# Kernel tuning notes

Measured on AMD Instinct MI355X. Metric: run time of the kernel, lower is better.

## Reference

```python
import jax, jax.numpy as jnp
import numpy as np

IN_FEATURES = 256
NUM_CENTERS = 4096
BATCH = 16384
SIGMA = 1.0


def setup_inputs() -> dict:
    key = jax.random.key(0)
    kx, kc, kw, kb = jax.random.split(key, 4)
    x = jax.random.normal(kx, (BATCH, IN_FEATURES), dtype=jnp.float32)
    centers = jax.random.normal(kc, (NUM_CENTERS, IN_FEATURES), dtype=jnp.float32)
    # nn.Linear(num_centers, 1) default init: U(-1/sqrt(fan_in), 1/sqrt(fan_in))
    bound = 1.0 / np.sqrt(NUM_CENTERS)
    w = jax.random.uniform(kw, (1, NUM_CENTERS), dtype=jnp.float32, minval=-bound, maxval=bound)
    b = jax.random.uniform(kb, (1,), dtype=jnp.float32, minval=-bound, maxval=bound)
    return {"x": x, "centers": centers, "w": w, "b": b}


def reference(x, centers, w, b):
    x_sq = jnp.sum(x * x, axis=1, keepdims=True)          # [B, 1]
    c_sq = jnp.sum(centers * centers, axis=1)             # [C]
    cross = jnp.einsum('bf,cf->bc', x, centers)           # [B, C]
    dist = x_sq + c_sq[None, :] - 2.0 * cross             # [B, C]
    phi = jnp.exp(-dist / (2.0 * SIGMA ** 2))             # [B, C]
    out = phi @ w.T + b                                   # [B, 1]
    return jax.nn.sigmoid(out)
```

## Files before the change

kernel.cpp:

```cpp
#include <hip/hip_runtime.h>
#include <hip/hip_bf16.h>


#define BATCH 16384
#define NCENT 4096
#define KDIM  256

using i32x4 = __attribute__((ext_vector_type(4))) int;

#define AS1 __attribute__((address_space(1)))
#define AS3 __attribute__((address_space(3)))
#define GLOAD_LDS16(g, l) \
  __builtin_amdgcn_global_load_lds((const AS1 void*)(g), (AS3 void*)(l), 16, 0, 0)

__device__ __forceinline__ unsigned short f2bf(float f) {
  unsigned int u = __float_as_uint(f);
  return (unsigned short)((u + 0x7FFFu + ((u >> 16) & 1u)) >> 16);
}

__device__ __forceinline__ signed char q16(float f) {
  int q = __float2int_rn(f * 16.0f);
  q = q > 127 ? 127 : (q < -127 ? -127 : q);
  return (signed char)q;
}

__global__ void rbf_prep(const float* __restrict__ x, const float* __restrict__ cent,
                         signed char* __restrict__ xq, signed char* __restrict__ cq,
                         float* __restrict__ xsq, float* __restrict__ csq,
                         float* __restrict__ part) {
  const int blk  = blockIdx.x;
  const int lane = threadIdx.x & 63;
  const int sub  = threadIdx.x >> 6;
  const float* src; signed char* dst; float* sq; int row;
  if (blk < BATCH / 4) {
    row = blk * 4 + sub; src = x; dst = xq; sq = xsq;
    if (threadIdx.x < 4) part[blk * 4 + threadIdx.x] = 0.f;
  } else {
    row = (blk - BATCH / 4) * 4 + sub; src = cent; dst = cq; sq = csq;
  }
  const float4 v = ((const float4*)(src + (size_t)row * KDIM))[lane];
  float s = v.x * v.x + v.y * v.y + v.z * v.z + v.w * v.w;
  char4 q = { q16(v.x), q16(v.y), q16(v.z), q16(v.w) };
  ((char4*)(dst + (size_t)row * KDIM))[lane] = q;
#pragma unroll
  for (int o = 32; o; o >>= 1) s += __shfl_xor(s, o);
  if (lane == 0) sq[row] = s;
}

__launch_bounds__(512, 2)
__global__ void rbf_main(const signed char* __restrict__ xq,
                         const signed char* __restrict__ cq,
                         const float* __restrict__ xsqg,
                         const float* __restrict__ csqg,
                         const float* __restrict__ w,
                         float* __restrict__ part) {
  __shared__ __align__(16) unsigned char Asm[128 * 256];
  __shared__ __align__(16) unsigned char Bb[3][256 * 64];
  __shared__ float xsqs[128], csqs[2048], wsh[2048], psum[128];
  __shared__ int sflag;

  const int bid = blockIdx.x;
  const int r0  = (bid >> 1) * 128;
  const int cb0 = (bid & 1) * 2048;

  const int tid = threadIdx.x;
  const int wid = tid >> 6, lane = tid & 63;
  const int wm  = wid >> 2, wn = wid & 3;
  const int lr  = lane & 15, kg = lane >> 4;

  if (tid < 128) { xsqs[tid] = 0.5f * xsqg[r0 + tid]; psum[tid] = 0.f; }
#pragma unroll
  for (int j = 0; j < 4; ++j) {
    csqs[tid + j * 512] = 0.5f * csqg[cb0 + tid + j * 512];
    wsh[tid + j * 512]  = w[cb0 + tid + j * 512];
  }
  if (tid == 0) sflag = 0;

  const int q1 = tid, q2 = tid + 512;
  const int p1 = (q1 & 7) ^ ((q1 >> 3) & 7);
  const int p2 = (q2 & 7) ^ ((q2 >> 3) & 7);
  const size_t bo1 = (size_t)((q1 >> 3) * 2 + (p1 >> 2)) * KDIM + (p1 & 3) * 16;
  const size_t bo2 = (size_t)((q2 >> 3) * 2 + (p2 >> 2)) * KDIM + (p2 & 3) * 16;
  const signed char* cqs = cq + (size_t)cb0 * KDIM;

  auto stageB = [&](int buf, int i) {
    const size_t base = (size_t)((i >> 2) * 256) * KDIM + (i & 3) * 64;
    GLOAD_LDS16(cqs + base + bo1, &Bb[buf][(wid * 64) * 16]);
    GLOAD_LDS16(cqs + base + bo2, &Bb[buf][(wid * 64 + 512) * 16]);
  };

#pragma unroll
  for (int j = 0; j < 4; ++j) {
    const int q = tid + j * 512;
    const int row = q >> 4, s = q & 15;
    GLOAD_LDS16(xq + (size_t)(r0 + row) * KDIM + ((s ^ (row & 15)) << 4),
                &Asm[(wid * 64 + j * 512) * 16]);
  }
  stageB(0, 0);
  stageB(1, 1);

  int arow[4], ax[4], boff[4];
#pragma unroll
  for (int m = 0; m < 4; ++m) {
    const int row = wm * 64 + m * 16 + lr;
    arow[m] = row * 256;
    ax[m]   = row & 15;
  }
#pragma unroll
  for (int n = 0; n < 4; ++n) {
    const int row = wn * 64 + n * 16 + lr;
    const int sr  = row >> 1;
    const int p   = ((row & 1) << 2) | kg;
    boff[n] = sr * 128 + (p ^ (sr & 7)) * 16;
  }

  asm volatile("s_waitcnt vmcnt(2) lgkmcnt(0)" ::: "memory");
  __builtin_amdgcn_s_barrier();

  i32x4 areg[4][4];
#pragma unroll
  for (int kst = 0; kst < 4; ++kst)
#pragma unroll
    for (int m = 0; m < 4; ++m)
      areg[kst][m] = *(const i32x4*)((const char*)Asm + arow[m] +
                                     (((kst * 4 + kg) ^ ax[m]) << 4));

  i32x4 acc[4][4];
#pragma unroll
  for (int m = 0; m < 4; ++m)
#pragma unroll
    for (int n = 0; n < 4; ++n)
      acc[m][n] = i32x4{0, 0, 0, 0};

  const float ISCL = 1.0f / 256.0f;

#pragma unroll
  for (int i = 0; i < 32; ++i) {
    const int kst = i & 3, tt = i >> 2;
    if (i > 0) {
      if (i < 31) asm volatile("s_waitcnt vmcnt(2)" ::: "memory");
      else        asm volatile("s_waitcnt vmcnt(0)" ::: "memory");
      __builtin_amdgcn_s_barrier();
    }

    i32x4 bf[4];
    const char* Bc = (const char*)&Bb[i % 3][0];
#pragma unroll
    for (int n = 0; n < 4; ++n)
      bf[n] = *(const i32x4*)(Bc + boff[n]);

    if (i <= 29) stageB((i + 2) % 3, i + 2);

    __builtin_amdgcn_s_setprio(1);
#pragma unroll
    for (int n = 0; n < 4; ++n)
#pragma unroll
      for (int m = 0; m < 4; ++m)
        acc[m][n] = __builtin_amdgcn_mfma_i32_16x16x64_i8(areg[kst][m], bf[n],
                                                          acc[m][n], 0, 0, 0);
    __builtin_amdgcn_s_setprio(0);

    if (kst == 3) {
      float hc[4], wc[4];
#pragma unroll
      for (int n = 0; n < 4; ++n) {
        const int colL = tt * 256 + wn * 64 + n * 16 + lr;
        hc[n] = csqs[colL]; wc[n] = wsh[colL];
      }
      float emax = -1e30f;
#pragma unroll
      for (int m = 0; m < 4; ++m)
#pragma unroll
        for (int r = 0; r < 4; ++r) {
          const float hx = xsqs[wm * 64 + m * 16 + kg * 4 + r];
#pragma unroll
          for (int n = 0; n < 4; ++n)
            emax = fmaxf(emax, (float)acc[m][n][r] * ISCL - hx - hc[n]);
        }
      if (!(bool)__all(emax < -30.0f)) {
        if (lane == 0) sflag = 1;
#pragma unroll
        for (int m = 0; m < 4; ++m)
#pragma unroll
          for (int r = 0; r < 4; ++r) {
            const float hx = xsqs[wm * 64 + m * 16 + kg * 4 + r];
            float v = 0.f;
#pragma unroll
            for (int n = 0; n < 4; ++n)
              v += wc[n] * __expf((float)acc[m][n][r] * ISCL - hx - hc[n]);
            v += __shfl_xor(v, 1);
            v += __shfl_xor(v, 2);
            v += __shfl_xor(v, 4);
            v += __shfl_xor(v, 8);
            if (lr == 0) atomicAdd(&psum[wm * 64 + m * 16 + kg * 4 + r], v);
          }
      }
#pragma unroll
      for (int m = 0; m < 4; ++m)
#pragma unroll
        for (int n = 0; n < 4; ++n)
          acc[m][n] = i32x4{0, 0, 0, 0};
    }
  }

  __syncthreads();
  if (sflag) {
    for (int t2 = tid; t2 < 128; t2 += 512) atomicAdd(&part[r0 + t2], psum[t2]);
  }
}

__global__ void rbf_finalize(float* __restrict__ part_out, const float* __restrict__ b, int n) {
  const int i = blockIdx.x * blockDim.x + threadIdx.x;
  if (i < n) {
    const float LOG2E = 1.44269504088896340736f;
    const float t = part_out[i] + b[0];
    part_out[i] = 1.0f / (1.0f + exp2f(-t * LOG2E));
  }
}

#define BM 128
#define BN 128
#define LDT 264

using f32x4 = __attribute__((ext_vector_type(4))) float;
using s16x8 = __attribute__((ext_vector_type(8))) short;

__launch_bounds__(512, 1)
__global__ void rbf_gemm_fb(const float* __restrict__ x,
                            const float* __restrict__ cent,
                            const float* __restrict__ w,
                            float* __restrict__ part) {
  __shared__ unsigned short As[BM][LDT];
  __shared__ unsigned short Bs[BN][LDT];
  __shared__ float xsq[BM], csq[BN], wsh[BN], psum[BM];

  const int tid = threadIdx.x;
  const int r0  = blockIdx.y * BM;
  const int c0  = blockIdx.x * BN;

  if (tid < BM) { xsq[tid] = 0.f; psum[tid] = 0.f; }
  else if (tid < BM + BN) { csq[tid - BM] = 0.f; }
  if (tid < BN) wsh[tid] = w[c0 + tid];
  __syncthreads();

  {
    const int row = tid >> 2, q = tid & 3;
    const float4* src = (const float4*)(x + (size_t)(r0 + row) * KDIM);
    float s = 0.f;
#pragma unroll
    for (int i = 0; i < 16; ++i) {
      const int c4 = q + 4 * i;
      float4 v = src[c4];
      s += v.x * v.x + v.y * v.y + v.z * v.z + v.w * v.w;
      ushort4 u = { f2bf(v.x), f2bf(v.y), f2bf(v.z), f2bf(v.w) };
      *(ushort4*)&As[row][c4 * 4] = u;
    }
    atomicAdd(&xsq[row], s);
  }
  {
    const int row = tid >> 2, q = tid & 3;
    const float4* src = (const float4*)(cent + (size_t)(c0 + row) * KDIM);
    float s = 0.f;
#pragma unroll
    for (int i = 0; i < 16; ++i) {
      const int c4 = q + 4 * i;
      float4 v = src[c4];
      s += v.x * v.x + v.y * v.y + v.z * v.z + v.w * v.w;
      ushort4 u = { f2bf(v.x), f2bf(v.y), f2bf(v.z), f2bf(v.w) };
      *(ushort4*)&Bs[row][c4 * 4] = u;
    }
    atomicAdd(&csq[row], s);
  }
  __syncthreads();

  const int wid = tid >> 6, lane = tid & 63;
  const int wm = wid >> 2, wn = wid & 3;
  const int lr = lane & 15, kg = lane >> 4;

  f32x4 acc[4][2];
#pragma unroll
  for (int m = 0; m < 4; ++m)
#pragma unroll
    for (int n = 0; n < 2; ++n)
      acc[m][n] = f32x4{0.f, 0.f, 0.f, 0.f};

#pragma unroll
  for (int ks = 0; ks < 8; ++ks) {
    const int kb = ks * 32 + kg * 8;
    s16x8 af[4], bfr[2];
#pragma unroll
    for (int m = 0; m < 4; ++m)
      af[m] = *(const s16x8*)&As[wm * 64 + m * 16 + lr][kb];
#pragma unroll
    for (int n = 0; n < 2; ++n)
      bfr[n] = *(const s16x8*)&Bs[wn * 32 + n * 16 + lr][kb];
#pragma unroll
    for (int m = 0; m < 4; ++m)
#pragma unroll
      for (int n = 0; n < 2; ++n)
        acc[m][n] = __builtin_amdgcn_mfma_f32_16x16x32_bf16(af[m], bfr[n], acc[m][n], 0, 0, 0);
  }

  const float LOG2E = 1.44269504088896340736f;
#pragma unroll
  for (int m = 0; m < 4; ++m) {
    const int rbase = wm * 64 + m * 16 + kg * 4;
#pragma unroll
    for (int r = 0; r < 4; ++r) {
      const float hxv = xsq[rbase + r];
      float v = 0.f;
#pragma unroll
      for (int n = 0; n < 2; ++n) {
        const int col = wn * 32 + n * 16 + lr;
        const float ev = acc[m][n][r] - 0.5f * (hxv + csq[col]);
        v += wsh[col] * exp2f(ev * LOG2E);
      }
      v += __shfl_xor(v, 1);
      v += __shfl_xor(v, 2);
      v += __shfl_xor(v, 4);
      v += __shfl_xor(v, 8);
      if (lr == 0) atomicAdd(&psum[rbase + r], v);
    }
  }
  __syncthreads();

  for (int t = tid; t < BM; t += 512) atomicAdd(&part[r0 + t], psum[t]);
}

extern "C" void kernel_launch(void* const* d_in, const int* in_sizes, int n_in,
                              void* d_out, int out_size, void* d_ws, size_t ws_size,
                              hipStream_t stream) {
  const float* x    = (const float*)d_in[0];
  const float* cent = (const float*)d_in[1];
  const float* w    = (const float*)d_in[2];
  const float* b    = (const float*)d_in[3];
  float* out = (float*)d_out;

  const size_t xq_off  = 0;
  const size_t cq_off  = (size_t)BATCH * KDIM;
  const size_t xsq_off = cq_off + (size_t)NCENT * KDIM;
  const size_t csq_off = xsq_off + (size_t)BATCH * 4;
  const size_t needed  = csq_off + (size_t)NCENT * 4;

  if (ws_size >= needed) {
    char* ws = (char*)d_ws;
    signed char* xqp = (signed char*)(ws + xq_off);
    signed char* cqp = (signed char*)(ws + cq_off);
    float* xsq = (float*)(ws + xsq_off);
    float* csq = (float*)(ws + csq_off);

    rbf_prep<<<BATCH / 4 + NCENT / 4, 256, 0, stream>>>(x, cent, xqp, cqp, xsq, csq, out);
    rbf_main<<<256, 512, 0, stream>>>(xqp, cqp, xsq, csq, w, out);
  } else {
    hipMemsetAsync(out, 0, (size_t)BATCH * sizeof(float), stream);
    dim3 grid(NCENT / BN, BATCH / BM);
    rbf_gemm_fb<<<grid, 512, 0, stream>>>(x, cent, w, out);
  }

  rbf_finalize<<<(BATCH + 255) / 256, 256, 0, stream>>>(out, b, BATCH);
}
```

Before: 31.41 us.

## Fuse x quantization and norm computation into main GEMM kernel

The prep kernel now quantizes only the centers. Each main-kernel block reads its 128 fp32 x rows directly, quantizes them to int8 into LDS with the swizzled layout, and computes the half squared norms in place. This removes the global int8 round trip for x and shrinks the prep grid. In exchange, the main kernel does more fp32 loads and conversion work before the first MFMA, and it now waits on all outstanding B loads (vmcnt(0)) before the barrier. The output-zeroing indexing in prep also changes from 4 to 16 entries per block.

```diff
diff --git a/kernel.cpp b/kernel.cpp
--- a/kernel.cpp
+++ b/kernel.cpp
@@ -24,33 +24,27 @@
   return (signed char)q;
 }
 
-__global__ void rbf_prep(const float* __restrict__ x, const float* __restrict__ cent,
-                         signed char* __restrict__ xq, signed char* __restrict__ cq,
-                         float* __restrict__ xsq, float* __restrict__ csq,
+__global__ void rbf_prep(const float* __restrict__ cent,
+                         signed char* __restrict__ cq,
+                         float* __restrict__ csq,
                          float* __restrict__ part) {
   const int blk  = blockIdx.x;
   const int lane = threadIdx.x & 63;
   const int sub  = threadIdx.x >> 6;
-  const float* src; signed char* dst; float* sq; int row;
-  if (blk < BATCH / 4) {
-    row = blk * 4 + sub; src = x; dst = xq; sq = xsq;
-    if (threadIdx.x < 4) part[blk * 4 + threadIdx.x] = 0.f;
-  } else {
-    row = (blk - BATCH / 4) * 4 + sub; src = cent; dst = cq; sq = csq;
-  }
-  const float4 v = ((const float4*)(src + (size_t)row * KDIM))[lane];
+  const int row  = blk * 4 + sub;
+  if (threadIdx.x < 16) part[blk * 16 + threadIdx.x] = 0.f;
+  const float4 v = ((const float4*)(cent + (size_t)row * KDIM))[lane];
   float s = v.x * v.x + v.y * v.y + v.z * v.z + v.w * v.w;
   char4 q = { q16(v.x), q16(v.y), q16(v.z), q16(v.w) };
-  ((char4*)(dst + (size_t)row * KDIM))[lane] = q;
+  ((char4*)(cq + (size_t)row * KDIM))[lane] = q;
 #pragma unroll
   for (int o = 32; o; o >>= 1) s += __shfl_xor(s, o);
-  if (lane == 0) sq[row] = s;
+  if (lane == 0) csq[row] = s;
 }
 
 __launch_bounds__(512, 2)
-__global__ void rbf_main(const signed char* __restrict__ xq,
+__global__ void rbf_main(const float* __restrict__ x,
                          const signed char* __restrict__ cq,
-                         const float* __restrict__ xsqg,
                          const float* __restrict__ csqg,
                          const float* __restrict__ w,
                          float* __restrict__ part) {
@@ -68,14 +62,6 @@
   const int wm  = wid >> 2, wn = wid & 3;
   const int lr  = lane & 15, kg = lane >> 4;
 
-  if (tid < 128) { xsqs[tid] = 0.5f * xsqg[r0 + tid]; psum[tid] = 0.f; }
-#pragma unroll
-  for (int j = 0; j < 4; ++j) {
-    csqs[tid + j * 512] = 0.5f * csqg[cb0 + tid + j * 512];
-    wsh[tid + j * 512]  = w[cb0 + tid + j * 512];
-  }
-  if (tid == 0) sflag = 0;
-
   const int q1 = tid, q2 = tid + 512;
   const int p1 = (q1 & 7) ^ ((q1 >> 3) & 7);
   const int p2 = (q2 & 7) ^ ((q2 >> 3) & 7);
@@ -89,15 +75,40 @@
     GLOAD_LDS16(cqs + base + bo2, &Bb[buf][(wid * 64 + 512) * 16]);
   };
 
-#pragma unroll
-  for (int j = 0; j < 4; ++j) {
-    const int q = tid + j * 512;
-    const int row = q >> 4, s = q & 15;
-    GLOAD_LDS16(xq + (size_t)(r0 + row) * KDIM + ((s ^ (row & 15)) << 4),
-                &Asm[(wid * 64 + j * 512) * 16]);
-  }
   stageB(0, 0);
   stageB(1, 1);
+
+  if (tid < 128) psum[tid] = 0.f;
+#pragma unroll
+  for (int j = 0; j < 4; ++j) {
+    csqs[tid + j * 512] = 0.5f * csqg[cb0 + tid + j * 512];
+    wsh[tid + j * 512]  = w[cb0 + tid + j * 512];
+  }
+  if (tid == 0) sflag = 0;
+
+  {
+    const int arowi = tid >> 2, aq = tid & 3;
+    const float4* srcA = (const float4*)(x + (size_t)(r0 + arowi) * KDIM) + aq * 16;
+    float s = 0.f;
+#pragma unroll
+    for (int j = 0; j < 4; ++j) {
+      unsigned int d[4];
+#pragma unroll
+      for (int k = 0; k < 4; ++k) {
+        const float4 v = srcA[j * 4 + k];
+        s += v.x * v.x + v.y * v.y + v.z * v.z + v.w * v.w;
+        d[k] = ((unsigned int)(unsigned char)q16(v.x)) |
+               ((unsigned int)(unsigned char)q16(v.y) << 8) |
+               ((unsigned int)(unsigned char)q16(v.z) << 16) |
+               ((unsigned int)(unsigned char)q16(v.w) << 24);
+      }
+      const int slot = (aq * 4 + j) ^ (arowi & 15);
+      *(uint4*)&Asm[arowi * 256 + slot * 16] = make_uint4(d[0], d[1], d[2], d[3]);
+    }
+    s += __shfl_xor(s, 1);
+    s += __shfl_xor(s, 2);
+    if (aq == 0) xsqs[arowi] = 0.5f * s;
+  }
 
   int arow[4], ax[4], boff[4];
 #pragma unroll
@@ -114,7 +125,7 @@
     boff[n] = sr * 128 + (p ^ (sr & 7)) * 16;
   }
 
-  asm volatile("s_waitcnt vmcnt(2) lgkmcnt(0)" ::: "memory");
+  asm volatile("s_waitcnt vmcnt(0) lgkmcnt(0)" ::: "memory");
   __builtin_amdgcn_s_barrier();
 
   i32x4 areg[4][4];
@@ -336,21 +347,17 @@
   const float* b    = (const float*)d_in[3];
   float* out = (float*)d_out;
 
-  const size_t xq_off  = 0;
-  const size_t cq_off  = (size_t)BATCH * KDIM;
-  const size_t xsq_off = cq_off + (size_t)NCENT * KDIM;
-  const size_t csq_off = xsq_off + (size_t)BATCH * 4;
+  const size_t cq_off  = 0;
+  const size_t csq_off = (size_t)NCENT * KDIM;
   const size_t needed  = csq_off + (size_t)NCENT * 4;
 
   if (ws_size >= needed) {
     char* ws = (char*)d_ws;
-    signed char* xqp = (signed char*)(ws + xq_off);
     signed char* cqp = (signed char*)(ws + cq_off);
-    float* xsq = (float*)(ws + xsq_off);
     float* csq = (float*)(ws + csq_off);
 
-    rbf_prep<<<BATCH / 4 + NCENT / 4, 256, 0, stream>>>(x, cent, xqp, cqp, xsq, csq, out);
-    rbf_main<<<256, 512, 0, stream>>>(xqp, cqp, xsq, csq, w, out);
+    rbf_prep<<<NCENT / 4, 256, 0, stream>>>(cent, cqp, csq, out);
+    rbf_main<<<256, 512, 0, stream>>>(x, cqp, csq, w, out);
   } else {
     hipMemsetAsync(out, 0, (size_t)BATCH * sizeof(float), stream);
     dim3 grid(NCENT / BN, BATCH / BM);
```

After: 39.48 us. +25.7%, slower.

## Process two B k-stages per barrier with a six-buffer, four-deep prefetch

Applied to the files above, without the earlier changes.

The main loop now handles two k-stages of the B tile per iteration, which halves the number of barriers and waits. The ring of LDS buffers for B grows from three to six, and the prefetch distance grows from two to four stages. This is meant to hide global-to-LDS latency better and to cut sync overhead. In exchange, LDS use rises by about 48KB, which may hurt the two-blocks-per-CU occupancy, and register pressure goes up from holding two B fragments at once.

```diff
diff --git a/kernel.cpp b/kernel.cpp
--- a/kernel.cpp
+++ b/kernel.cpp
@@ -55,7 +55,7 @@
                          const float* __restrict__ w,
                          float* __restrict__ part) {
   __shared__ __align__(16) unsigned char Asm[128 * 256];
-  __shared__ __align__(16) unsigned char Bb[3][256 * 64];
+  __shared__ __align__(16) unsigned char Bb[6][256 * 64];
   __shared__ float xsqs[128], csqs[2048], wsh[2048], psum[128];
   __shared__ int sflag;
 
@@ -83,8 +83,8 @@
   const size_t bo2 = (size_t)((q2 >> 3) * 2 + (p2 >> 2)) * KDIM + (p2 & 3) * 16;
   const signed char* cqs = cq + (size_t)cb0 * KDIM;
 
-  auto stageB = [&](int buf, int i) {
-    const size_t base = (size_t)((i >> 2) * 256) * KDIM + (i & 3) * 64;
+  auto stageB = [&](int buf, int s) {
+    const size_t base = (size_t)((s >> 2) * 256) * KDIM + (s & 3) * 64;
     GLOAD_LDS16(cqs + base + bo1, &Bb[buf][(wid * 64) * 16]);
     GLOAD_LDS16(cqs + base + bo2, &Bb[buf][(wid * 64 + 512) * 16]);
   };
@@ -98,6 +98,8 @@
   }
   stageB(0, 0);
   stageB(1, 1);
+  stageB(2, 2);
+  stageB(3, 3);
 
   int arow[4], ax[4], boff[4];
 #pragma unroll
@@ -114,7 +116,7 @@
     boff[n] = sr * 128 + (p ^ (sr & 7)) * 16;
   }
 
-  asm volatile("s_waitcnt vmcnt(2) lgkmcnt(0)" ::: "memory");
+  asm volatile("s_waitcnt vmcnt(8) lgkmcnt(0)" ::: "memory");
   __builtin_amdgcn_s_barrier();
 
   i32x4 areg[4][4];
@@ -135,32 +137,46 @@
   const float ISCL = 1.0f / 256.0f;
 
 #pragma unroll
-  for (int i = 0; i < 32; ++i) {
-    const int kst = i & 3, tt = i >> 2;
-    if (i > 0) {
-      if (i < 31) asm volatile("s_waitcnt vmcnt(2)" ::: "memory");
+  for (int j = 0; j < 16; ++j) {
+    const int s0 = 2 * j, s1 = 2 * j + 1;
+    if (j > 0) {
+      if (j < 15) asm volatile("s_waitcnt vmcnt(4)" ::: "memory");
       else        asm volatile("s_waitcnt vmcnt(0)" ::: "memory");
       __builtin_amdgcn_s_barrier();
     }
 
-    i32x4 bf[4];
-    const char* Bc = (const char*)&Bb[i % 3][0];
+    i32x4 bf0[4], bf1[4];
+    const char* Bc0 = (const char*)&Bb[s0 % 6][0];
+    const char* Bc1 = (const char*)&Bb[s1 % 6][0];
+#pragma unroll
+    for (int n = 0; n < 4; ++n) {
+      bf0[n] = *(const i32x4*)(Bc0 + boff[n]);
+      bf1[n] = *(const i32x4*)(Bc1 + boff[n]);
+    }
+
+    if (j <= 13) {
+      stageB((s0 + 4) % 6, s0 + 4);
+      stageB((s1 + 4) % 6, s1 + 4);
+    }
+
+    const int k0 = s0 & 3;
+    __builtin_amdgcn_s_setprio(1);
 #pragma unroll
     for (int n = 0; n < 4; ++n)
-      bf[n] = *(const i32x4*)(Bc + boff[n]);
-
-    if (i <= 29) stageB((i + 2) % 3, i + 2);
-
-    __builtin_amdgcn_s_setprio(1);
+#pragma unroll
+      for (int m = 0; m < 4; ++m)
+        acc[m][n] = __builtin_amdgcn_mfma_i32_16x16x64_i8(areg[k0][m], bf0[n],
+                                                          acc[m][n], 0, 0, 0);
 #pragma unroll
     for (int n = 0; n < 4; ++n)
 #pragma unroll
       for (int m = 0; m < 4; ++m)
-        acc[m][n] = __builtin_amdgcn_mfma_i32_16x16x64_i8(areg[kst][m], bf[n],
+        acc[m][n] = __builtin_amdgcn_mfma_i32_16x16x64_i8(areg[k0 + 1][m], bf1[n],
                                                           acc[m][n], 0, 0, 0);
     __builtin_amdgcn_s_setprio(0);
 
-    if (kst == 3) {
+    if ((s1 & 3) == 3) {
+      const int tt = s1 >> 2;
       float hc[4], wc[4];
 #pragma unroll
       for (int n = 0; n < 4; ++n) {
```

After: 30.79 us (median of 2 runs). -2.0%, faster.

## Load A fragments directly to registers and stage B in full-K double buffers

Applied to the files above, without the earlier changes.

Drops the shared-memory A tile and loads the int8 x fragments straight from global into registers. LDS is reused for an 8-slot B buffer, so each iteration stages a whole 256-column, full-K tile (four k-steps) as one half of a double buffer. The loop becomes 8 iterations with 64 MFMAs each and one barrier per tile instead of per k-step. The aim is fewer barriers and waits per unit of work. In exchange each wait drains all outstanding loads (vmcnt(0)), and register pressure rises from holding 16 B fragments at once.

```diff
diff --git a/kernel.cpp b/kernel.cpp
--- a/kernel.cpp
+++ b/kernel.cpp
@@ -54,8 +54,7 @@
                          const float* __restrict__ csqg,
                          const float* __restrict__ w,
                          float* __restrict__ part) {
-  __shared__ __align__(16) unsigned char Asm[128 * 256];
-  __shared__ __align__(16) unsigned char Bb[3][256 * 64];
+  __shared__ __align__(16) unsigned char Bb[8][256 * 64];
   __shared__ float xsqs[128], csqs[2048], wsh[2048], psum[128];
   __shared__ int sflag;
 
@@ -68,13 +67,13 @@
   const int wm  = wid >> 2, wn = wid & 3;
   const int lr  = lane & 15, kg = lane >> 4;
 
-  if (tid < 128) { xsqs[tid] = 0.5f * xsqg[r0 + tid]; psum[tid] = 0.f; }
-#pragma unroll
-  for (int j = 0; j < 4; ++j) {
-    csqs[tid + j * 512] = 0.5f * csqg[cb0 + tid + j * 512];
-    wsh[tid + j * 512]  = w[cb0 + tid + j * 512];
-  }
-  if (tid == 0) sflag = 0;
+  i32x4 areg[4][4];
+#pragma unroll
+  for (int kst = 0; kst < 4; ++kst)
+#pragma unroll
+    for (int m = 0; m < 4; ++m)
+      areg[kst][m] = *(const i32x4*)(xq + (size_t)(r0 + wm * 64 + m * 16 + lr) * KDIM
+                                        + (kst * 4 + kg) * 16);
 
   const int q1 = tid, q2 = tid + 512;
   const int p1 = (q1 & 7) ^ ((q1 >> 3) & 7);
@@ -83,29 +82,26 @@
   const size_t bo2 = (size_t)((q2 >> 3) * 2 + (p2 >> 2)) * KDIM + (p2 & 3) * 16;
   const signed char* cqs = cq + (size_t)cb0 * KDIM;
 
-  auto stageB = [&](int buf, int i) {
-    const size_t base = (size_t)((i >> 2) * 256) * KDIM + (i & 3) * 64;
+  auto stageB = [&](int buf, int s) {
+    const size_t base = (size_t)((s >> 2) * 256) * KDIM + (s & 3) * 64;
     GLOAD_LDS16(cqs + base + bo1, &Bb[buf][(wid * 64) * 16]);
     GLOAD_LDS16(cqs + base + bo2, &Bb[buf][(wid * 64 + 512) * 16]);
   };
 
-#pragma unroll
-  for (int j = 0; j < 4; ++j) {
-    const int q = tid + j * 512;
-    const int row = q >> 4, s = q & 15;
-    GLOAD_LDS16(xq + (size_t)(r0 + row) * KDIM + ((s ^ (row & 15)) << 4),
-                &Asm[(wid * 64 + j * 512) * 16]);
-  }
   stageB(0, 0);
   stageB(1, 1);
-
-  int arow[4], ax[4], boff[4];
-#pragma unroll
-  for (int m = 0; m < 4; ++m) {
-    const int row = wm * 64 + m * 16 + lr;
-    arow[m] = row * 256;
-    ax[m]   = row & 15;
-  }
+  stageB(2, 2);
+  stageB(3, 3);
+
+  if (tid < 128) { xsqs[tid] = 0.5f * xsqg[r0 + tid]; psum[tid] = 0.f; }
+#pragma unroll
+  for (int j = 0; j < 4; ++j) {
+    csqs[tid + j * 512] = 0.5f * csqg[cb0 + tid + j * 512];
+    wsh[tid + j * 512]  = w[cb0 + tid + j * 512];
+  }
+  if (tid == 0) sflag = 0;
+
+  int boff[4];
 #pragma unroll
   for (int n = 0; n < 4; ++n) {
     const int row = wn * 64 + n * 16 + lr;
@@ -114,16 +110,8 @@
     boff[n] = sr * 128 + (p ^ (sr & 7)) * 16;
   }
 
-  asm volatile("s_waitcnt vmcnt(2) lgkmcnt(0)" ::: "memory");
+  asm volatile("s_waitcnt vmcnt(0) lgkmcnt(0)" ::: "memory");
   __builtin_amdgcn_s_barrier();
-
-  i32x4 areg[4][4];
-#pragma unroll
-  for (int kst = 0; kst < 4; ++kst)
-#pragma unroll
-    for (int m = 0; m < 4; ++m)
-      areg[kst][m] = *(const i32x4*)((const char*)Asm + arow[m] +
-                                     (((kst * 4 + kg) ^ ax[m]) << 4));
 
   i32x4 acc[4][4];
 #pragma unroll
@@ -135,36 +123,45 @@
   const float ISCL = 1.0f / 256.0f;
 
 #pragma unroll
-  for (int i = 0; i < 32; ++i) {
-    const int kst = i & 3, tt = i >> 2;
-    if (i > 0) {
-      if (i < 31) asm volatile("s_waitcnt vmcnt(2)" ::: "memory");
-      else        asm volatile("s_waitcnt vmcnt(0)" ::: "memory");
+  for (int j = 0; j < 8; ++j) {
+    if (j > 0) {
+      asm volatile("s_waitcnt vmcnt(0)" ::: "memory");
       __builtin_amdgcn_s_barrier();
     }
 
-    i32x4 bf[4];
-    const char* Bc = (const char*)&Bb[i % 3][0];
-#pragma unroll
-    for (int n = 0; n < 4; ++n)
-      bf[n] = *(const i32x4*)(Bc + boff[n]);
-
-    if (i <= 29) stageB((i + 2) % 3, i + 2);
+    i32x4 bf[4][4];
+    const int half = (j & 1) * 4;
+#pragma unroll
+    for (int ss = 0; ss < 4; ++ss) {
+      const char* Bc = (const char*)&Bb[half + ss][0];
+#pragma unroll
+      for (int n = 0; n < 4; ++n)
+        bf[ss][n] = *(const i32x4*)(Bc + boff[n]);
+    }
+
+    if (j < 7) {
+      const int oh = ((j + 1) & 1) * 4;
+#pragma unroll
+      for (int ss = 0; ss < 4; ++ss)
+        stageB(oh + ss, 4 * (j + 1) + ss);
+    }
 
     __builtin_amdgcn_s_setprio(1);
 #pragma unroll
-    for (int n = 0; n < 4; ++n)
-#pragma unroll
-      for (int m = 0; m < 4; ++m)
-        acc[m][n] = __builtin_amdgcn_mfma_i32_16x16x64_i8(areg[kst][m], bf[n],
-                                                          acc[m][n], 0, 0, 0);
+    for (int ss = 0; ss < 4; ++ss)
+#pragma unroll
+      for (int n = 0; n < 4; ++n)
+#pragma unroll
+        for (int m = 0; m < 4; ++m)
+          acc[m][n] = __builtin_amdgcn_mfma_i32_16x16x64_i8(areg[ss][m], bf[ss][n],
+                                                            acc[m][n], 0, 0, 0);
     __builtin_amdgcn_s_setprio(0);
 
-    if (kst == 3) {
+    {
       float hc[4], wc[4];
 #pragma unroll
       for (int n = 0; n < 4; ++n) {
-        const int colL = tt * 256 + wn * 64 + n * 16 + lr;
+        const int colL = j * 256 + wn * 64 + n * 16 + lr;
         hc[n] = csqs[colL]; wc[n] = wsh[colL];
       }
       float emax = -1e30f;
```

New measurement: 34.22 us. +8.9%, slower.
